# Kernel tuning notes

Measured on AMD Instinct MI355X. Metric: run time of the kernel, lower is better.

The kernel has to match this reference:

```python
import jax, jax.numpy as jnp
import numpy as np

B, S, D, H = 2, 2048, 1024, 16
DK = D // H
NEG = -1e9


def setup_inputs() -> dict:
    key = jax.random.key(0)
    ks = jax.random.split(key, 12)
    inp = {
        "query": jax.random.normal(ks[0], (B, S, D), jnp.float32),
        "key": jax.random.normal(ks[1], (B, S, D), jnp.float32),
        "value": jax.random.normal(ks[2], (B, S, D), jnp.float32),
        "mask": jax.random.randint(ks[3], (B, S), 0, 2, jnp.int32),
    }
    # 4 linears (q, k, v, out), each d_model x d_model with bias.
    scale = 1.0 / np.sqrt(D)
    for i, name in enumerate(["wq", "wk", "wv", "wo"]):
        inp[name] = jax.random.uniform(ks[4 + i], (D, D), jnp.float32, -scale, scale)
        inp["b" + name[1]] = jax.random.uniform(ks[8 + i], (D,), jnp.float32, -scale, scale)
    return inp


def _split_heads(x):  # [B,S,D] -> [B,H,S,DK]
    return x.reshape(B, S, H, DK).transpose(0, 2, 1, 3)


def reference(query, key, value, mask, wq, bq, wk, bk, wv, bv, wo, bo):
    q = _split_heads(query @ wq.T + bq)
    k = _split_heads(key @ wk.T + bk)
    v = _split_heads(value @ wv.T + bv)
    scores = jnp.einsum("bhqd,bhkd->bhqk", q, k) / jnp.sqrt(jnp.float32(DK))
    # mask: [B,S] -> [B,1,1,S]; masked_fill where mask == 0
    m = mask[:, None, None, :]
    scores = jnp.where(m == 0, NEG, scores)
    attn = jax.nn.softmax(scores, axis=-1)  # dropout p=0 (eval) -> identity
    x = jnp.einsum("bhqk,bhkd->bhqd", attn, v)
    x = x.transpose(0, 2, 1, 3).reshape(B, S, D)
    return x @ wo.T + bo
```

## Files before the change

### kernel.cpp

```cpp
#include <hip/hip_runtime.h>


typedef _Float16 f16;
typedef _Float16 f16x8 __attribute__((ext_vector_type(8)));
typedef _Float16 f16x4 __attribute__((ext_vector_type(4)));
typedef __fp16 fp16x2r __attribute__((ext_vector_type(2)));
typedef float f32x4 __attribute__((ext_vector_type(4)));

union F16x4u { f16x4 v; fp16x2r h[2]; };

#define MFMA_F16(a, b, c) __builtin_amdgcn_mfma_f32_16x16x32_f16((a), (b), (c), 0, 0, 0)
#define MFMA16(a, b, c) __builtin_amdgcn_mfma_f32_16x16x16f16((a), (b), (c), 0, 0, 0)
#define L2E 1.44269504088896340736f

__device__ __forceinline__ void gld16(const void* g, void* l) {
    __builtin_amdgcn_global_load_lds(
        (__attribute__((address_space(1))) void*)(g),
        (__attribute__((address_space(3))) void*)(l), 16, 0, 0);
}

__global__ __launch_bounds__(256) void cvt_kernel(
    const float* __restrict__ q, const float* __restrict__ k,
    const float* __restrict__ v,
    const float* __restrict__ wq, const float* __restrict__ wk,
    const float* __restrict__ wv, const float* __restrict__ wo,
    f16* __restrict__ oq, f16* __restrict__ ok, f16* __restrict__ ov,
    f16* __restrict__ owq, f16* __restrict__ owk, f16* __restrict__ owv,
    f16* __restrict__ owo)
{
    const int z = blockIdx.y;
    const float* src;
    f16* dst;
    int n;
    switch (z) {
        case 0: src = q;  dst = oq;  n = 4194304; break;
        case 1: src = k;  dst = ok;  n = 4194304; break;
        case 2: src = v;  dst = ov;  n = 4194304; break;
        case 3: src = wq; dst = owq; n = 1048576; break;
        case 4: src = wk; dst = owk; n = 1048576; break;
        case 5: src = wv; dst = owv; n = 1048576; break;
        default: src = wo; dst = owo; n = 1048576; break;
    }
    int idx = (blockIdx.x * 256 + threadIdx.x) * 8;
    if (idx >= n) return;
    float4 a = *(const float4*)(src + idx);
    float4 b = *(const float4*)(src + idx + 4);
    f16x8 h = { (f16)a.x, (f16)a.y, (f16)a.z, (f16)a.w,
                (f16)b.x, (f16)b.y, (f16)b.z, (f16)b.w };
    *(f16x8*)(dst + idx) = h;
}

__global__ __launch_bounds__(256) void proj_qkv_kernel(
    const f16* __restrict__ xq, const f16* __restrict__ xk,
    const f16* __restrict__ xv,
    const f16* __restrict__ wqh, const f16* __restrict__ wkh,
    const f16* __restrict__ wvh,
    const float* __restrict__ bq, const float* __restrict__ bk,
    const float* __restrict__ bv,
    f16* __restrict__ qh, f16* __restrict__ kh, f16* __restrict__ vt)
{
    const int z = blockIdx.z;
    const f16* X = (z == 0) ? xq : (z == 1) ? xk : xv;
    const f16* W = (z == 0) ? wqh : (z == 1) ? wkh : wvh;
    const float* bias = (z == 0) ? bq : (z == 1) ? bk : bv;
    const f16* P0 = (z < 2) ? W : X;
    const f16* P1 = (z < 2) ? X : W;

    __shared__ __align__(16) f16 As[128 * 64];
    __shared__ __align__(16) f16 Bs[128 * 64];

    const int t = threadIdx.x;
    const int wave = t >> 6, lane = t & 63, quad = lane >> 4, l15 = lane & 15;
    const int m_base = (wave >> 1) * 64, n_base = (wave & 1) * 64;
    const int blockM = (z < 2) ? blockIdx.y * 128 : blockIdx.x * 128;
    const int blockN = (z < 2) ? blockIdx.x * 128 : blockIdx.y * 128;

    const int srow = lane >> 3;
    const int sblk = (lane & 7) ^ srow;

    f32x4 acc[4][4];
#pragma unroll
    for (int mt = 0; mt < 4; mt++)
#pragma unroll
        for (int nt = 0; nt < 4; nt++)
            acc[mt][nt] = (f32x4){0.f, 0.f, 0.f, 0.f};

    for (int k0 = 0; k0 < 1024; k0 += 64) {
        __syncthreads();
#pragma unroll
        for (int j = 0; j < 4; j++) {
            int r0 = wave * 32 + j * 8;
            gld16(&P0[(size_t)(blockM + r0 + srow) * 1024 + k0 + sblk * 8],
                  &As[r0 * 64]);
            gld16(&P1[(size_t)(blockN + r0 + srow) * 1024 + k0 + sblk * 8],
                  &Bs[r0 * 64]);
        }
        __syncthreads();

#pragma unroll
        for (int c = 0; c < 2; c++) {
            f16x8 af[4], bf[4];
#pragma unroll
            for (int mt = 0; mt < 4; mt++)
                af[mt] = *(const f16x8*)(&As[(m_base + mt * 16 + l15) * 64 +
                                             (((c * 4 + quad) ^ (l15 & 7)) << 3)]);
#pragma unroll
            for (int nt = 0; nt < 4; nt++)
                bf[nt] = *(const f16x8*)(&Bs[(n_base + nt * 16 + l15) * 64 +
                                             (((c * 4 + quad) ^ (l15 & 7)) << 3)]);
#pragma unroll
            for (int mt = 0; mt < 4; mt++)
#pragma unroll
                for (int nt = 0; nt < 4; nt++)
                    acc[mt][nt] = MFMA_F16(af[mt], bf[nt], acc[mt][nt]);
        }
    }

    if (z < 2) {
        f16* o = (z == 0) ? qh : kh;
        const float scale = (z == 0) ? 0.125f * L2E : 1.0f;
#pragma unroll
        for (int mt = 0; mt < 4; mt++) {
            int j0 = blockM + m_base + mt * 16 + quad * 4;
            float4 b4 = *(const float4*)(&bias[j0]);
            int h = j0 >> 6, dk = j0 & 63;
#pragma unroll
            for (int nt = 0; nt < 4; nt++) {
                int s_g = blockN + n_base + nt * 16 + l15;
                int b = s_g >> 11, s = s_g & 2047;
                f16x4 pk = { (f16)((acc[mt][nt][0] + b4.x) * scale),
                             (f16)((acc[mt][nt][1] + b4.y) * scale),
                             (f16)((acc[mt][nt][2] + b4.z) * scale),
                             (f16)((acc[mt][nt][3] + b4.w) * scale) };
                *(f16x4*)(&o[(((size_t)(b * 16 + h) * 2048 + s) << 6) + dk]) = pk;
            }
        }
    } else {
        float bv_[4];
#pragma unroll
        for (int nt = 0; nt < 4; nt++)
            bv_[nt] = bias[blockN + n_base + nt * 16 + l15];
#pragma unroll
        for (int mt = 0; mt < 4; mt++) {
            int row0 = blockM + m_base + mt * 16 + quad * 4;
            int b = row0 >> 11, s0 = row0 & 2047;
#pragma unroll
            for (int nt = 0; nt < 4; nt++) {
                int col_g = blockN + n_base + nt * 16 + l15;
                int h = col_g >> 6, dk = col_g & 63;
                f16x4 pk = { (f16)(acc[mt][nt][0] + bv_[nt]),
                             (f16)(acc[mt][nt][1] + bv_[nt]),
                             (f16)(acc[mt][nt][2] + bv_[nt]),
                             (f16)(acc[mt][nt][3] + bv_[nt]) };
                *(f16x4*)(&vt[((size_t)((b * 16 + h) * 64 + dk) << 11) + s0]) = pk;
            }
        }
    }
}

__global__ __launch_bounds__(256) void flash_kernel(
    const f16* __restrict__ qh, const f16* __restrict__ kh,
    const f16* __restrict__ vt, const int* __restrict__ mask,
    f16* __restrict__ ctx)
{
    __shared__ __align__(16) f16 Ks[2][64 * 64];
    __shared__ __align__(16) f16 Vts[2][64 * 64];
    __shared__ float bias_all[2048];

    const int t = threadIdx.x;
    const int wave = t >> 6, lane = t & 63, quad = lane >> 4, l15 = lane & 15;
    const int bh = blockIdx.x;
    const int b = bh >> 4, h = bh & 15;
    const int q0 = blockIdx.y * 128;

    const f16* qbase = qh + (size_t)bh * (2048 * 64);
    const f16* kbase = kh + (size_t)bh * (2048 * 64);
    const f16* vbase = vt + (size_t)bh * (64 * 2048);

#pragma unroll
    for (int j = 0; j < 8; j++) {
        int i = j * 256 + t;
        bias_all[i] = (mask[b * 2048 + i] == 0) ? -1.0e9f : 0.0f;
    }

    f16x8 qf[2][2];
#pragma unroll
    for (int cb = 0; cb < 2; cb++) {
        int qrow = q0 + wave * 32 + cb * 16 + l15;
        qf[cb][0] = *(const f16x8*)(&qbase[qrow * 64 + quad * 8]);
        qf[cb][1] = *(const f16x8*)(&qbase[qrow * 64 + 32 + quad * 8]);
    }

    f32x4 O[2][4];
#pragma unroll
    for (int cb = 0; cb < 2; cb++)
#pragma unroll
        for (int n = 0; n < 4; n++) O[cb][n] = (f32x4){0.f, 0.f, 0.f, 0.f};
    float l_part[2] = {0.f, 0.f};

    const int srow8 = lane >> 3;
    const int sblk = (lane & 7) ^ srow8;

#pragma unroll
    for (int p = 0; p < 2; p++) {
        int r0 = p * 32 + wave * 8;
        int row = r0 + srow8;
        gld16(&kbase[(size_t)row * 64 + sblk * 8], &Ks[0][r0 * 64]);
        gld16(&vbase[(size_t)row * 2048 + sblk * 8], &Vts[0][r0 * 64]);
    }

    for (int kt = 0; kt < 32; kt++) {
        const int cur = kt & 1;
        __syncthreads();

        if (kt < 31) {
            const int key0n = (kt + 1) * 64;
#pragma unroll
            for (int p = 0; p < 2; p++) {
                int r0 = p * 32 + wave * 8;
                int row = r0 + srow8;
                gld16(&kbase[(size_t)(key0n + row) * 64 + sblk * 8],
                      &Ks[cur ^ 1][r0 * 64]);
                gld16(&vbase[(size_t)row * 2048 + key0n + sblk * 8],
                      &Vts[cur ^ 1][r0 * 64]);
            }
        }

        const int key0 = kt * 64;
        f32x4 sc[2][4];
#pragma unroll
        for (int nt = 0; nt < 4; nt++) {
            const f16* krow = &Ks[cur][(nt * 16 + l15) * 64];
            f16x8 kf0 = *(const f16x8*)(&krow[(quad ^ (l15 & 7)) << 3]);
            f16x8 kf1 = *(const f16x8*)(&krow[((quad + 4) ^ (l15 & 7)) << 3]);
            float4 b4 = *(const float4*)(&bias_all[key0 + nt * 16 + quad * 4]);
#pragma unroll
            for (int cb = 0; cb < 2; cb++) {
                f32x4 z4 = (f32x4){b4.x, b4.y, b4.z, b4.w};
                z4 = MFMA_F16(kf0, qf[cb][0], z4);
                sc[cb][nt] = MFMA_F16(kf1, qf[cb][1], z4);
            }
        }

        f16x4 pf[2][4];
#pragma unroll
        for (int cb = 0; cb < 2; cb++) {
            float rs = 0.f;
#pragma unroll
            for (int nt = 0; nt < 4; nt++) {
                float p0 = exp2f(sc[cb][nt][0]);
                float p1 = exp2f(sc[cb][nt][1]);
                float p2 = exp2f(sc[cb][nt][2]);
                float p3 = exp2f(sc[cb][nt][3]);
                rs += (p0 + p1) + (p2 + p3);
                F16x4u u;
                u.h[0] = __builtin_amdgcn_cvt_pkrtz(p0, p1);
                u.h[1] = __builtin_amdgcn_cvt_pkrtz(p2, p3);
                pf[cb][nt] = u.v;
            }
            l_part[cb] += rs;
        }

#pragma unroll
        for (int nto = 0; nto < 4; nto++) {
            const f16* vrow = &Vts[cur][(nto * 16 + l15) * 64];
#pragma unroll
            for (int nt = 0; nt < 4; nt++) {
                f16x4 vf = *(const f16x4*)(&vrow[
                    (((nt * 2 + (quad >> 1)) ^ (l15 & 7)) << 3) + (quad & 1) * 4]);
                O[0][nto] = MFMA16(vf, pf[0][nt], O[0][nto]);
                O[1][nto] = MFMA16(vf, pf[1][nt], O[1][nto]);
            }
        }
    }

#pragma unroll
    for (int cb = 0; cb < 2; cb++) {
        float l = l_part[cb];
        l += __shfl_xor(l, 16);
        l += __shfl_xor(l, 32);
        const float inv_l = 1.0f / l;
        int qrow = q0 + wave * 32 + cb * 16 + l15;
#pragma unroll
        for (int nto = 0; nto < 4; nto++) {
            f16x4 pk = { (f16)(O[cb][nto][0] * inv_l),
                         (f16)(O[cb][nto][1] * inv_l),
                         (f16)(O[cb][nto][2] * inv_l),
                         (f16)(O[cb][nto][3] * inv_l) };
            *(f16x4*)(&ctx[(size_t)(b * 2048 + qrow) * 1024 + h * 64 +
                           nto * 16 + quad * 4]) = pk;
        }
    }
}

__global__ __launch_bounds__(256) void proj_out_kernel(
    const f16* __restrict__ ctx, const f16* __restrict__ woh,
    const float* __restrict__ bo, float* __restrict__ out)
{
    __shared__ __align__(16) f16 As[2][128 * 64];
    __shared__ __align__(16) f16 Bs[2][64 * 64];

    const int t = threadIdx.x;
    const int wave = t >> 6, lane = t & 63, quad = lane >> 4, l15 = lane & 15;
    const int m_base = (wave >> 1) * 64, n_base = (wave & 1) * 32;
    const int blockM = blockIdx.x * 128;
    const int blockN = blockIdx.y * 64;

    const int srow = lane >> 3;
    const int sblk = (lane & 7) ^ srow;

    f32x4 acc[4][2];
#pragma unroll
    for (int mt = 0; mt < 4; mt++)
#pragma unroll
        for (int nt = 0; nt < 2; nt++)
            acc[mt][nt] = (f32x4){0.f, 0.f, 0.f, 0.f};

#pragma unroll
    for (int j = 0; j < 4; j++) {
        int r0 = wave * 32 + j * 8;
        gld16(&ctx[(size_t)(blockM + r0 + srow) * 1024 + sblk * 8],
              &As[0][r0 * 64]);
    }
#pragma unroll
    for (int j = 0; j < 2; j++) {
        int r0 = wave * 16 + j * 8;
        gld16(&woh[(size_t)(blockN + r0 + srow) * 1024 + sblk * 8],
              &Bs[0][r0 * 64]);
    }

    for (int ki = 0; ki < 16; ki++) {
        const int cur = ki & 1;
        __syncthreads();

        if (ki < 15) {
            const int k0n = (ki + 1) * 64;
#pragma unroll
            for (int j = 0; j < 4; j++) {
                int r0 = wave * 32 + j * 8;
                gld16(&ctx[(size_t)(blockM + r0 + srow) * 1024 + k0n + sblk * 8],
                      &As[cur ^ 1][r0 * 64]);
            }
#pragma unroll
            for (int j = 0; j < 2; j++) {
                int r0 = wave * 16 + j * 8;
                gld16(&woh[(size_t)(blockN + r0 + srow) * 1024 + k0n + sblk * 8],
                      &Bs[cur ^ 1][r0 * 64]);
            }
        }

#pragma unroll
        for (int c = 0; c < 2; c++) {
            f16x8 af[4], bf[2];
#pragma unroll
            for (int mt = 0; mt < 4; mt++)
                af[mt] = *(const f16x8*)(&As[cur][(m_base + mt * 16 + l15) * 64 +
                                              (((c * 4 + quad) ^ (l15 & 7)) << 3)]);
#pragma unroll
            for (int nt = 0; nt < 2; nt++)
                bf[nt] = *(const f16x8*)(&Bs[cur][(n_base + nt * 16 + l15) * 64 +
                                              (((c * 4 + quad) ^ (l15 & 7)) << 3)]);
#pragma unroll
            for (int mt = 0; mt < 4; mt++)
#pragma unroll
                for (int nt = 0; nt < 2; nt++)
                    acc[mt][nt] = MFMA_F16(af[mt], bf[nt], acc[mt][nt]);
        }
    }

    float bo_[2];
#pragma unroll
    for (int nt = 0; nt < 2; nt++)
        bo_[nt] = bo[blockN + n_base + nt * 16 + l15];

#pragma unroll
    for (int mt = 0; mt < 4; mt++) {
        int row0 = blockM + m_base + mt * 16 + quad * 4;
#pragma unroll
        for (int nt = 0; nt < 2; nt++) {
            int col_g = blockN + n_base + nt * 16 + l15;
#pragma unroll
            for (int i = 0; i < 4; i++)
                out[(size_t)(row0 + i) * 1024 + col_g] = acc[mt][nt][i] + bo_[nt];
        }
    }
}

extern "C" void kernel_launch(void* const* d_in, const int* in_sizes, int n_in,
                              void* d_out, int out_size, void* d_ws, size_t ws_size,
                              hipStream_t stream) {
    const float* query = (const float*)d_in[0];
    const float* key_  = (const float*)d_in[1];
    const float* value = (const float*)d_in[2];
    const int*   mask  = (const int*)d_in[3];
    const float* wq = (const float*)d_in[4];
    const float* bq = (const float*)d_in[5];
    const float* wk = (const float*)d_in[6];
    const float* bk = (const float*)d_in[7];
    const float* wv = (const float*)d_in[8];
    const float* bv = (const float*)d_in[9];
    const float* wo = (const float*)d_in[10];
    const float* bo = (const float*)d_in[11];
    float* out = (float*)d_out;

    f16* xq  = (f16*)d_ws;
    f16* xk  = xq  + 4194304;
    f16* xv  = xk  + 4194304;
    f16* wqh = xv  + 4194304;
    f16* wkh = wqh + 1048576;
    f16* wvh = wkh + 1048576;
    f16* woh = wvh + 1048576;
    f16* qh  = woh + 1048576;
    f16* kh  = qh  + 4194304;
    f16* vt  = kh  + 4194304;
    f16* ctx = xq;

    cvt_kernel<<<dim3(2048, 7), 256, 0, stream>>>(
        query, key_, value, wq, wk, wv, wo, xq, xk, xv, wqh, wkh, wvh, woh);
    proj_qkv_kernel<<<dim3(32, 8, 3), 256, 0, stream>>>(
        xq, xk, xv, wqh, wkh, wvh, bq, bk, bv, qh, kh, vt);
    flash_kernel<<<dim3(32, 16), 256, 0, stream>>>(qh, kh, vt, mask, ctx);
    proj_out_kernel<<<dim3(32, 16), 256, 0, stream>>>(ctx, woh, bo, out);
}
```

Measured before the change: 242.4 us.

## Stage QKV projection epilogue through LDS for coalesced stores; MFMA row sums in flash

The Q/K and V projection epilogues now write results into a shared-memory tile and then emit 16-byte coalesced global stores, replacing scattered 8-byte stores. In the flash kernel the double-buffered loop is unrolled into two explicit phases with separate buffers. The softmax row sum is now accumulated with an MFMA against a ones vector, which removes the scalar adds and the final cross-lane shuffles. These changes add extra barriers in the epilogue and extra MFMA work per tile in exchange.

```diff
diff --git a/kernel.cpp b/kernel.cpp
--- a/kernel.cpp
+++ b/kernel.cpp
@@ -66,8 +66,10 @@
     const f16* P0 = (z < 2) ? W : X;
     const f16* P1 = (z < 2) ? X : W;
 
-    __shared__ __align__(16) f16 As[128 * 64];
-    __shared__ __align__(16) f16 Bs[128 * 64];
+    __shared__ __align__(16) f16 smem[16384];
+    f16* As = smem;
+    f16* Bs = smem + 8192;
+    f16* L  = smem;
 
     const int t = threadIdx.x;
     const int wave = t >> 6, lane = t & 63, quad = lane >> 4, l15 = lane & 15;
@@ -119,20 +121,39 @@
     if (z < 2) {
         f16* o = (z == 0) ? qh : kh;
         const float scale = (z == 0) ? 0.125f * L2E : 1.0f;
-#pragma unroll
-        for (int mt = 0; mt < 4; mt++) {
-            int j0 = blockM + m_base + mt * 16 + quad * 4;
-            float4 b4 = *(const float4*)(&bias[j0]);
-            int h = j0 >> 6, dk = j0 & 63;
-#pragma unroll
-            for (int nt = 0; nt < 4; nt++) {
-                int s_g = blockN + n_base + nt * 16 + l15;
-                int b = s_g >> 11, s = s_g & 2047;
-                f16x4 pk = { (f16)((acc[mt][nt][0] + b4.x) * scale),
-                             (f16)((acc[mt][nt][1] + b4.y) * scale),
-                             (f16)((acc[mt][nt][2] + b4.z) * scale),
-                             (f16)((acc[mt][nt][3] + b4.w) * scale) };
-                *(f16x4*)(&o[(((size_t)(b * 16 + h) * 2048 + s) << 6) + dk]) = pk;
+        float4 b4[4];
+#pragma unroll
+        for (int mt = 0; mt < 4; mt++)
+            b4[mt] = *(const float4*)(&bias[blockM + m_base + mt * 16 + quad * 4]);
+
+#pragma unroll
+        for (int half = 0; half < 2; half++) {
+            __syncthreads();
+            if ((wave & 1) == half) {
+#pragma unroll
+                for (int mt = 0; mt < 4; mt++)
+#pragma unroll
+                    for (int nt = 0; nt < 4; nt++) {
+                        f16x4 pk = {
+                            (f16)((acc[mt][nt][0] + b4[mt].x) * scale),
+                            (f16)((acc[mt][nt][1] + b4[mt].y) * scale),
+                            (f16)((acc[mt][nt][2] + b4[mt].z) * scale),
+                            (f16)((acc[mt][nt][3] + b4[mt].w) * scale) };
+                        *(f16x4*)(&L[(nt * 16 + l15) * 136 +
+                                     m_base + mt * 16 + quad * 4]) = pk;
+                    }
+            }
+            __syncthreads();
+#pragma unroll
+            for (int pass = 0; pass < 4; pass++) {
+                int unit = pass * 32 + (t >> 3);
+                int hh = unit >> 6, s_loc = unit & 63;
+                f16x8 vv = *(const f16x8*)(&L[s_loc * 136 + hh * 64 + (t & 7) * 8]);
+                int s_glob = blockN + half * 64 + s_loc;
+                int b = s_glob >> 11, s = s_glob & 2047;
+                int h_glob = (blockM >> 6) + hh;
+                *(f16x8*)(&o[(((size_t)(b * 16 + h_glob) * 2048 + s) << 6) +
+                             (t & 7) * 8]) = vv;
             }
         }
     } else {
@@ -140,20 +161,95 @@
 #pragma unroll
         for (int nt = 0; nt < 4; nt++)
             bv_[nt] = bias[blockN + n_base + nt * 16 + l15];
-#pragma unroll
-        for (int mt = 0; mt < 4; mt++) {
-            int row0 = blockM + m_base + mt * 16 + quad * 4;
-            int b = row0 >> 11, s0 = row0 & 2047;
-#pragma unroll
-            for (int nt = 0; nt < 4; nt++) {
-                int col_g = blockN + n_base + nt * 16 + l15;
-                int h = col_g >> 6, dk = col_g & 63;
-                f16x4 pk = { (f16)(acc[mt][nt][0] + bv_[nt]),
-                             (f16)(acc[mt][nt][1] + bv_[nt]),
-                             (f16)(acc[mt][nt][2] + bv_[nt]),
-                             (f16)(acc[mt][nt][3] + bv_[nt]) };
-                *(f16x4*)(&vt[((size_t)((b * 16 + h) * 64 + dk) << 11) + s0]) = pk;
-            }
+
+#pragma unroll
+        for (int half = 0; half < 2; half++) {
+            __syncthreads();
+            if ((wave & 1) == half) {
+#pragma unroll
+                for (int mt = 0; mt < 4; mt++)
+#pragma unroll
+                    for (int nt = 0; nt < 4; nt++) {
+                        f16x4 pk = { (f16)(acc[mt][nt][0] + bv_[nt]),
+                                     (f16)(acc[mt][nt][1] + bv_[nt]),
+                                     (f16)(acc[mt][nt][2] + bv_[nt]),
+                                     (f16)(acc[mt][nt][3] + bv_[nt]) };
+                        *(f16x4*)(&L[(nt * 16 + l15) * 136 +
+                                     m_base + mt * 16 + quad * 4]) = pk;
+                    }
+            }
+            __syncthreads();
+#pragma unroll
+            for (int pass = 0; pass < 4; pass++) {
+                int f_loc = pass * 16 + (t >> 4);
+                f16x8 vv = *(const f16x8*)(&L[f_loc * 136 + (t & 15) * 8]);
+                int feat = blockN + half * 64 + f_loc;
+                int hh = feat >> 6, dk = feat & 63;
+                int b = blockM >> 11;
+                int s0 = (blockM & 2047) + (t & 15) * 8;
+                *(f16x8*)(&vt[((size_t)((b * 16 + hh) * 64 + dk) << 11) + s0]) = vv;
+            }
+        }
+    }
+}
+
+__device__ __forceinline__ void flash_stage(
+    const f16* kbase, const f16* vbase, int key0,
+    f16* Kb, f16* Vb, int wave, int srow8, int sblk)
+{
+#pragma unroll
+    for (int p = 0; p < 2; p++) {
+        int r0 = p * 32 + wave * 8;
+        int row = r0 + srow8;
+        gld16(&kbase[(size_t)(key0 + row) * 64 + sblk * 8], &Kb[r0 * 64]);
+        gld16(&vbase[(size_t)row * 2048 + key0 + sblk * 8], &Vb[r0 * 64]);
+    }
+}
+
+__device__ __forceinline__ void flash_phase(
+    const f16* Kbuf, const f16* Vbuf, const float* bias_all, int key0,
+    const f16x8 (&qf)[2][2], int quad, int l15,
+    f32x4 (&O)[2][4], f32x4 (&lacc)[2])
+{
+    f32x4 sc[2][4];
+#pragma unroll
+    for (int nt = 0; nt < 4; nt++) {
+        const f16* krow = &Kbuf[(nt * 16 + l15) * 64];
+        f16x8 kf0 = *(const f16x8*)(&krow[(quad ^ (l15 & 7)) << 3]);
+        f16x8 kf1 = *(const f16x8*)(&krow[((quad + 4) ^ (l15 & 7)) << 3]);
+        float4 b4 = *(const float4*)(&bias_all[key0 + nt * 16 + quad * 4]);
+#pragma unroll
+        for (int cb = 0; cb < 2; cb++) {
+            f32x4 z4 = (f32x4){b4.x, b4.y, b4.z, b4.w};
+            z4 = MFMA_F16(kf0, qf[cb][0], z4);
+            sc[cb][nt] = MFMA_F16(kf1, qf[cb][1], z4);
+        }
+    }
+    const f16x4 ones = {(f16)1.f, (f16)1.f, (f16)1.f, (f16)1.f};
+    f16x4 pf[2][4];
+#pragma unroll
+    for (int cb = 0; cb < 2; cb++)
+#pragma unroll
+        for (int nt = 0; nt < 4; nt++) {
+            float p0 = exp2f(sc[cb][nt][0]);
+            float p1 = exp2f(sc[cb][nt][1]);
+            float p2 = exp2f(sc[cb][nt][2]);
+            float p3 = exp2f(sc[cb][nt][3]);
+            F16x4u u;
+            u.h[0] = __builtin_amdgcn_cvt_pkrtz(p0, p1);
+            u.h[1] = __builtin_amdgcn_cvt_pkrtz(p2, p3);
+            pf[cb][nt] = u.v;
+            lacc[cb] = MFMA16(ones, pf[cb][nt], lacc[cb]);
+        }
+#pragma unroll
+    for (int nto = 0; nto < 4; nto++) {
+        const f16* vrow = &Vbuf[(nto * 16 + l15) * 64];
+#pragma unroll
+        for (int nt = 0; nt < 4; nt++) {
+            f16x4 vf = *(const f16x4*)(&vrow[
+                (((nt * 2 + (quad >> 1)) ^ (l15 & 7)) << 3) + (quad & 1) * 4]);
+            O[0][nto] = MFMA16(vf, pf[0][nt], O[0][nto]);
+            O[1][nto] = MFMA16(vf, pf[1][nt], O[1][nto]);
         }
     }
 }
@@ -163,8 +259,10 @@
     const f16* __restrict__ vt, const int* __restrict__ mask,
     f16* __restrict__ ctx)
 {
-    __shared__ __align__(16) f16 Ks[2][64 * 64];
-    __shared__ __align__(16) f16 Vts[2][64 * 64];
+    __shared__ __align__(16) f16 Ks0[64 * 64];
+    __shared__ __align__(16) f16 Ks1[64 * 64];
+    __shared__ __align__(16) f16 Vts0[64 * 64];
+    __shared__ __align__(16) f16 Vts1[64 * 64];
     __shared__ float bias_all[2048];
 
     const int t = threadIdx.x;
@@ -196,90 +294,27 @@
     for (int cb = 0; cb < 2; cb++)
 #pragma unroll
         for (int n = 0; n < 4; n++) O[cb][n] = (f32x4){0.f, 0.f, 0.f, 0.f};
-    float l_part[2] = {0.f, 0.f};
+    f32x4 lacc[2] = {(f32x4){0.f, 0.f, 0.f, 0.f}, (f32x4){0.f, 0.f, 0.f, 0.f}};
 
     const int srow8 = lane >> 3;
     const int sblk = (lane & 7) ^ srow8;
 
-#pragma unroll
-    for (int p = 0; p < 2; p++) {
-        int r0 = p * 32 + wave * 8;
-        int row = r0 + srow8;
-        gld16(&kbase[(size_t)row * 64 + sblk * 8], &Ks[0][r0 * 64]);
-        gld16(&vbase[(size_t)row * 2048 + sblk * 8], &Vts[0][r0 * 64]);
-    }
-
-    for (int kt = 0; kt < 32; kt++) {
-        const int cur = kt & 1;
+    flash_stage(kbase, vbase, 0, Ks0, Vts0, wave, srow8, sblk);
+
+    for (int k2 = 0; k2 < 16; k2++) {
+        const int key0 = k2 * 128;
         __syncthreads();
-
-        if (kt < 31) {
-            const int key0n = (kt + 1) * 64;
-#pragma unroll
-            for (int p = 0; p < 2; p++) {
-                int r0 = p * 32 + wave * 8;
-                int row = r0 + srow8;
-                gld16(&kbase[(size_t)(key0n + row) * 64 + sblk * 8],
-                      &Ks[cur ^ 1][r0 * 64]);
-                gld16(&vbase[(size_t)row * 2048 + key0n + sblk * 8],
-                      &Vts[cur ^ 1][r0 * 64]);
-            }
-        }
-
-        const int key0 = kt * 64;
-        f32x4 sc[2][4];
-#pragma unroll
-        for (int nt = 0; nt < 4; nt++) {
-            const f16* krow = &Ks[cur][(nt * 16 + l15) * 64];
-            f16x8 kf0 = *(const f16x8*)(&krow[(quad ^ (l15 & 7)) << 3]);
-            f16x8 kf1 = *(const f16x8*)(&krow[((quad + 4) ^ (l15 & 7)) << 3]);
-            float4 b4 = *(const float4*)(&bias_all[key0 + nt * 16 + quad * 4]);
-#pragma unroll
-            for (int cb = 0; cb < 2; cb++) {
-                f32x4 z4 = (f32x4){b4.x, b4.y, b4.z, b4.w};
-                z4 = MFMA_F16(kf0, qf[cb][0], z4);
-                sc[cb][nt] = MFMA_F16(kf1, qf[cb][1], z4);
-            }
-        }
-
-        f16x4 pf[2][4];
-#pragma unroll
-        for (int cb = 0; cb < 2; cb++) {
-            float rs = 0.f;
-#pragma unroll
-            for (int nt = 0; nt < 4; nt++) {
-                float p0 = exp2f(sc[cb][nt][0]);
-                float p1 = exp2f(sc[cb][nt][1]);
-                float p2 = exp2f(sc[cb][nt][2]);
-                float p3 = exp2f(sc[cb][nt][3]);
-                rs += (p0 + p1) + (p2 + p3);
-                F16x4u u;
-                u.h[0] = __builtin_amdgcn_cvt_pkrtz(p0, p1);
-                u.h[1] = __builtin_amdgcn_cvt_pkrtz(p2, p3);
-                pf[cb][nt] = u.v;
-            }
-            l_part[cb] += rs;
-        }
-
-#pragma unroll
-        for (int nto = 0; nto < 4; nto++) {
-            const f16* vrow = &Vts[cur][(nto * 16 + l15) * 64];
-#pragma unroll
-            for (int nt = 0; nt < 4; nt++) {
-                f16x4 vf = *(const f16x4*)(&vrow[
-                    (((nt * 2 + (quad >> 1)) ^ (l15 & 7)) << 3) + (quad & 1) * 4]);
-                O[0][nto] = MFMA16(vf, pf[0][nt], O[0][nto]);
-                O[1][nto] = MFMA16(vf, pf[1][nt], O[1][nto]);
-            }
-        }
+        flash_stage(kbase, vbase, key0 + 64, Ks1, Vts1, wave, srow8, sblk);
+        flash_phase(Ks0, Vts0, bias_all, key0, qf, quad, l15, O, lacc);
+        __syncthreads();
+        if (k2 < 15)
+            flash_stage(kbase, vbase, key0 + 128, Ks0, Vts0, wave, srow8, sblk);
+        flash_phase(Ks1, Vts1, bias_all, key0 + 64, qf, quad, l15, O, lacc);
     }
 
 #pragma unroll
     for (int cb = 0; cb < 2; cb++) {
-        float l = l_part[cb];
-        l += __shfl_xor(l, 16);
-        l += __shfl_xor(l, 32);
-        const float inv_l = 1.0f / l;
+        const float inv_l = 1.0f / lacc[cb][0];
         int qrow = q0 + wave * 32 + cb * 16 + l15;
 #pragma unroll
         for (int nto = 0; nto < 4; nto++) {
```

New measurement: 236.2 us. 2.5% less time.
